# Kernel tuning notes

Hardware: AMD Instinct MI355X
Metric: run time of the kernel (lower is better)

## Reference

```python
import jax, jax.numpy as jnp
import numpy as np

D_MODEL = 1024
N_HEADS = 16
D_K = D_MODEL // N_HEADS
D_FF = 4096
B = 2
T = 2048


def _layernorm(x, gamma, beta, eps=1e-5):
    mu = jnp.mean(x, axis=-1, keepdims=True)
    var = jnp.var(x, axis=-1, keepdims=True)
    return (x - mu) * jax.lax.rsqrt(var + eps) * gamma + beta


def _attention(q_in, kv_in, Wq, bq, Wk, bk, Wv, bv, mask):
    # q_in: [B,Tq,D], kv_in: [B,Tk,D]; Wq/Wk/Wv: [H,D,d_k]; b*: [H,d_k]
    Q = jnp.einsum('btd,hdk->bhtk', q_in, Wq) + bq[None, :, None, :]
    K = jnp.einsum('bsd,hdk->bhsk', kv_in, Wk) + bk[None, :, None, :]
    V = jnp.einsum('bsd,hdk->bhsk', kv_in, Wv) + bv[None, :, None, :]
    scores = jnp.einsum('bhtk,bhsk->bhts', Q, K) / jnp.sqrt(jnp.asarray(D_K, Q.dtype))
    if mask is not None:
        scores = jnp.where(mask, scores, jnp.finfo(scores.dtype).min)
    attn = jax.nn.softmax(scores, axis=-1)
    out = jnp.einsum('bhts,bhsk->bhtk', attn, V)  # [B,H,Tq,d_k]
    # concat heads: [B,Tq,H*d_k] == [B,Tq,D]
    return out.transpose(0, 2, 1, 3).reshape(q_in.shape[0], q_in.shape[1], -1)


def setup_inputs() -> dict:
    key = jax.random.key(0)
    ks = jax.random.split(key, 24)
    s = 0.02
    inp = {
        'dec_input': jax.random.normal(ks[0], (B, T, D_MODEL), jnp.float32),
        'enc_output': jax.random.normal(ks[1], (B, T, D_MODEL), jnp.float32),
        # self-attention per-head weights stacked over heads
        'Wq_s': jax.random.normal(ks[2], (N_HEADS, D_MODEL, D_K), jnp.float32) * s,
        'bq_s': jnp.zeros((N_HEADS, D_K), jnp.float32),
        'Wk_s': jax.random.normal(ks[3], (N_HEADS, D_MODEL, D_K), jnp.float32) * s,
        'bk_s': jnp.zeros((N_HEADS, D_K), jnp.float32),
        'Wv_s': jax.random.normal(ks[4], (N_HEADS, D_MODEL, D_K), jnp.float32) * s,
        'bv_s': jnp.zeros((N_HEADS, D_K), jnp.float32),
        'Wo_s': jax.random.normal(ks[5], (D_MODEL, D_MODEL), jnp.float32) * s,
        'bo_s': jnp.zeros((D_MODEL,), jnp.float32),
        # cross-attention per-head weights
        'Wq_c': jax.random.normal(ks[6], (N_HEADS, D_MODEL, D_K), jnp.float32) * s,
        'bq_c': jnp.zeros((N_HEADS, D_K), jnp.float32),
        'Wk_c': jax.random.normal(ks[7], (N_HEADS, D_MODEL, D_K), jnp.float32) * s,
        'bk_c': jnp.zeros((N_HEADS, D_K), jnp.float32),
        'Wv_c': jax.random.normal(ks[8], (N_HEADS, D_MODEL, D_K), jnp.float32) * s,
        'bv_c': jnp.zeros((N_HEADS, D_K), jnp.float32),
        'Wo_c': jax.random.normal(ks[9], (D_MODEL, D_MODEL), jnp.float32) * s,
        'bo_c': jnp.zeros((D_MODEL,), jnp.float32),
        # FFN
        'W1': jax.random.normal(ks[10], (D_MODEL, D_FF), jnp.float32) * s,
        'b1': jnp.zeros((D_FF,), jnp.float32),
        'W2': jax.random.normal(ks[11], (D_FF, D_MODEL), jnp.float32) * s,
        'b2': jnp.zeros((D_MODEL,), jnp.float32),
        # layernorms
        'g1': jnp.ones((D_MODEL,), jnp.float32), 'be1': jnp.zeros((D_MODEL,), jnp.float32),
        'g2': jnp.ones((D_MODEL,), jnp.float32), 'be2': jnp.zeros((D_MODEL,), jnp.float32),
        'g3': jnp.ones((D_MODEL,), jnp.float32), 'be3': jnp.zeros((D_MODEL,), jnp.float32),
    }
    return inp


def reference(dec_input, enc_output,
              Wq_s, bq_s, Wk_s, bk_s, Wv_s, bv_s, Wo_s, bo_s,
              Wq_c, bq_c, Wk_c, bk_c, Wv_c, bv_c, Wo_c, bo_c,
              W1, b1, W2, b2, g1, be1, g2, be2, g3, be3):
    Tq = dec_input.shape[1]
    causal = jnp.tril(jnp.ones((Tq, Tq), bool))[None, None, :, :]  # [1,1,T,T]
    # masked multi-head self-attention (dropout is identity in eval)
    sa = _attention(dec_input, dec_input, Wq_s, bq_s, Wk_s, bk_s, Wv_s, bv_s, causal)
    sa = sa @ Wo_s.T if False else jnp.einsum('btd,ed->bte', sa, Wo_s.T) if False else sa @ Wo_s + bo_s
    x1 = _layernorm(dec_input + sa, g1, be1)
    # cross-attention (no mask)
    ca = _attention(x1, enc_output, Wq_c, bq_c, Wk_c, bk_c, Wv_c, bv_c, None)
    ca = ca @ Wo_c + bo_c
    x2 = _layernorm(x1 + ca, g2, be2)
    # FFN
    ffn = jax.nn.relu(x2 @ W1 + b1) @ W2 + b2
    x3 = _layernorm(x2 + ffn, g3, be3)
    return x3
```

## Files before the change

kernel.cpp:

```cpp
#include <hip/hip_runtime.h>
#include <hip/hip_bf16.h>

typedef __attribute__((ext_vector_type(8))) short short8;
typedef __attribute__((ext_vector_type(4))) short short4v;
typedef __attribute__((ext_vector_type(4))) float floatx4;

#define TDIM 2048
#define BDIM 2
#define MROWS (BDIM * TDIM)

#define ASM_VMCNT0() __asm__ volatile("s_waitcnt vmcnt(0)" ::: "memory")
#define ASM_VMCNT2() __asm__ volatile("s_waitcnt vmcnt(2)" ::: "memory")
#define ASM_LGKM0()  __asm__ volatile("s_waitcnt lgkmcnt(0)" ::: "memory")
#define ASM_BARRIER() __asm__ volatile("s_barrier" ::: "memory")

__device__ __forceinline__ floatx4 mfma16(short4v a, short4v b, floatx4 c) {
#if defined(__HIP_DEVICE_COMPILE__)
#if __has_builtin(__builtin_amdgcn_mfma_f32_16x16x16bf16_1k)
    return __builtin_amdgcn_mfma_f32_16x16x16bf16_1k(a, b, c, 0, 0, 0);
#else
    short8 az = {a[0], a[1], a[2], a[3], 0, 0, 0, 0};
    short8 bz = {b[0], b[1], b[2], b[3], 0, 0, 0, 0};
    return __builtin_amdgcn_mfma_f32_16x16x32_bf16(az, bz, c, 0, 0, 0);
#endif
#else
    (void)a; (void)b;
    return c;
#endif
}

__device__ __forceinline__ void gload_lds16(const void* g, void* l) {
    __builtin_amdgcn_global_load_lds((const __attribute__((address_space(1))) void*)g,
                                     (__attribute__((address_space(3))) void*)l, 16, 0, 0);
}

__device__ __forceinline__ short bf16s(float x) {
    __hip_bfloat16 h = __float2bfloat16(x);
    return *(short*)&h;
}

__device__ __forceinline__ float fexp2(float x) {
#if defined(__HIP_DEVICE_COMPILE__)
#if __has_builtin(__builtin_amdgcn_exp2f)
    return __builtin_amdgcn_exp2f(x);
#else
    return exp2f(x);
#endif
#else
    return x;
#endif
}

__global__ __launch_bounds__(256) void cast2_k(const float* __restrict__ a,
                                               const float* __restrict__ b,
                                               __hip_bfloat16* __restrict__ oa,
                                               __hip_bfloat16* __restrict__ ob) {
    const int blk = blockIdx.x;
    const float* in = (blk < 4096) ? a : b;
    __hip_bfloat16* out = (blk < 4096) ? oa : ob;
    const size_t base = (size_t)(blk & 4095) * 1024 + threadIdx.x * 4;
    float4 v = *(const float4*)&in[base];
    out[base + 0] = __float2bfloat16(v.x);
    out[base + 1] = __float2bfloat16(v.y);
    out[base + 2] = __float2bfloat16(v.z);
    out[base + 3] = __float2bfloat16(v.w);
}

__device__ __forceinline__ void t32(float (*tile)[33], const float* __restrict__ in,
                                    __hip_bfloat16* __restrict__ out, int R, int C,
                                    int c0, int r0) {
    const int tx = threadIdx.x & 31, ty = threadIdx.x >> 5;
#pragma unroll
    for (int i = 0; i < 4; ++i)
        tile[ty + 8 * i][tx] = in[(size_t)(r0 + ty + 8 * i) * C + c0 + tx];
    __syncthreads();
#pragma unroll
    for (int i = 0; i < 4; ++i)
        out[(size_t)(c0 + ty + 8 * i) * R + r0 + tx] = __float2bfloat16(tile[tx][ty + 8 * i]);
}

__global__ __launch_bounds__(256) void prep_w_k(
    const float* __restrict__ Wq_s, const float* __restrict__ Wk_s, const float* __restrict__ Wv_s,
    const float* __restrict__ Wq_c, const float* __restrict__ Wk_c, const float* __restrict__ Wv_c,
    const float* __restrict__ Wo_s, const float* __restrict__ Wo_c,
    const float* __restrict__ W1, const float* __restrict__ W2,
    const float* __restrict__ bq_s, const float* __restrict__ bk_s, const float* __restrict__ bv_s,
    const float* __restrict__ bk_c, const float* __restrict__ bv_c,
    __hip_bfloat16* __restrict__ WtQKVs, __hip_bfloat16* __restrict__ WtQc,
    __hip_bfloat16* __restrict__ WtKVc, __hip_bfloat16* __restrict__ WtOs,
    __hip_bfloat16* __restrict__ WtOc, __hip_bfloat16* __restrict__ Wt1,
    __hip_bfloat16* __restrict__ Wt2,
    float* __restrict__ BiasQKVs, float* __restrict__ BiasKVc) {
    __shared__ float tile[32][33];
    const int t = blockIdx.x;
    if (t < 6144) {
        const int seg = t >> 10, tl = t & 1023;
        const float* s;
        __hip_bfloat16* d;
        if (seg == 0) { s = Wq_s; d = WtQKVs; }
        else if (seg == 1) { s = Wk_s; d = WtQKVs + 1048576; }
        else if (seg == 2) { s = Wv_s; d = WtQKVs + 2097152; }
        else if (seg == 3) { s = Wq_c; d = WtQc; }
        else if (seg == 4) { s = Wk_c; d = WtKVc; }
        else { s = Wv_c; d = WtKVc + 1048576; }
        const int slab = tl >> 6, rem = tl & 63;
        t32(tile, s + (size_t)slab * 65536, d + (size_t)slab * 65536, 1024, 64,
            (rem & 1) * 32, (rem >> 1) * 32);
    } else if (t < 8192) {
        const int rem = (t - 6144) & 1023;
        const float* s = (t < 7168) ? Wo_s : Wo_c;
        __hip_bfloat16* d = (t < 7168) ? WtOs : WtOc;
        t32(tile, s, d, 1024, 1024, (rem & 31) * 32, (rem >> 5) * 32);
    } else if (t < 12288) {
        const int rem = t - 8192;
        t32(tile, W1, Wt1, 1024, 4096, (rem & 127) * 32, (rem >> 7) * 32);
    } else if (t < 16384) {
        const int rem = t - 12288;
        t32(tile, W2, Wt2, 4096, 1024, (rem & 31) * 32, (rem >> 5) * 32);
    } else if (t < 16396) {
        const int i = (t - 16384) * 256 + threadIdx.x;
        BiasQKVs[i] = (i < 1024) ? bq_s[i] : (i < 2048 ? bk_s[i - 1024] : bv_s[i - 2048]);
    } else {
        const int i = (t - 16396) * 256 + threadIdx.x;
        BiasKVc[i] = (i < 1024) ? bk_c[i] : bv_c[i - 1024];
    }
}

__device__ __forceinline__ void gemm_core(
    const __hip_bfloat16* __restrict__ A, const __hip_bfloat16* __restrict__ Bt,
    int K, int kBeg, int kLen,
    const float* __restrict__ bias, __hip_bfloat16* __restrict__ C, int ldc,
    float* __restrict__ Pf,
    __hip_bfloat16* __restrict__ Vt, int vt_col0, int relu,
    int m0, int n0, __hip_bfloat16* sm) {
    const int tid = threadIdx.x;
    const int lane = tid & 63, wave = tid >> 6;
    const int quad = lane >> 4, l16 = lane & 15;
    const int wm = (wave >> 1) * 64, wn = (wave & 1) * 64;
    const int lrow = lane >> 3;
    const int gsw = (((lane & 7) ^ lrow)) * 8;
    const int sw7 = l16 & 7;
    const __hip_bfloat16* gA = A + (size_t)(m0 + wave * 32 + lrow) * K + kBeg + gsw;
    const __hip_bfloat16* gB = Bt + (size_t)(n0 + wave * 32 + lrow) * K + kBeg + gsw;
    __hip_bfloat16* lA = sm + wave * 2048;
    __hip_bfloat16* lB = sm + 16384 + wave * 2048;
    floatx4 acc[4][4] = {};
    const int T = kLen >> 6;
#pragma unroll
    for (int i = 0; i < 4; ++i) {
        gload_lds16(gA + (size_t)i * 8 * K, lA + i * 512);
        gload_lds16(gB + (size_t)i * 8 * K, lB + i * 512);
    }
    for (int t = 0; t < T; ++t) {
        ASM_VMCNT0();
        ASM_BARRIER();
        if (t + 1 < T) {
            const int koff = (t + 1) << 6;
            const int b = ((t + 1) & 1) * 8192;
#pragma unroll
            for (int i = 0; i < 4; ++i) {
                gload_lds16(gA + (size_t)i * 8 * K + koff, lA + b + i * 512);
                gload_lds16(gB + (size_t)i * 8 * K + koff, lB + b + i * 512);
            }
        }
        const __hip_bfloat16* cA = sm + (t & 1) * 8192;
        const __hip_bfloat16* cB = sm + 16384 + (t & 1) * 8192;
#pragma unroll
        for (int kc = 0; kc < 2; ++kc) {
            short8 af[4], bfr[4];
#pragma unroll
            for (int i = 0; i < 4; ++i) {
                af[i] = *(const short8*)&cA[(wm + i * 16 + l16) * 64 +
                                            (((kc * 4 + quad) ^ sw7) * 8)];
                bfr[i] = *(const short8*)&cB[(wn + i * 16 + l16) * 64 +
                                             (((kc * 4 + quad) ^ sw7) * 8)];
            }
#pragma unroll
            for (int mi = 0; mi < 4; ++mi)
#pragma unroll
                for (int ni = 0; ni < 4; ++ni)
                    acc[mi][ni] =
                        __builtin_amdgcn_mfma_f32_16x16x32_bf16(af[mi], bfr[ni], acc[mi][ni], 0, 0, 0);
        }
    }
    if (Pf) {
#pragma unroll
        for (int ni = 0; ni < 4; ++ni) {
            const int col = n0 + wn + ni * 16 + l16;
#pragma unroll
            for (int mi = 0; mi < 4; ++mi)
#pragma unroll
                for (int r = 0; r < 4; ++r) {
                    const int row = m0 + wm + mi * 16 + quad * 4 + r;
                    Pf[(size_t)row * ldc + col] = acc[mi][ni][r];
                }
        }
    } else {
        const bool toVt = (n0 >= vt_col0);
#pragma unroll
        for (int ni = 0; ni < 4; ++ni) {
            const int col = n0 + wn + ni * 16 + l16;
            const float bv = bias[col];
#pragma unroll
            for (int mi = 0; mi < 4; ++mi) {
                const int row0 = m0 + wm + mi * 16 + quad * 4;
                if (toVt) {
                    const int b = row0 >> 11, t0 = row0 & (TDIM - 1);
                    short4v pk;
#pragma unroll
                    for (int r = 0; r < 4; ++r) pk[r] = bf16s(acc[mi][ni][r] + bv);
                    *(short4v*)&Vt[((size_t)(b * 1024 + (col - vt_col0)) << 11) + t0] = pk;
                } else {
#pragma unroll
                    for (int r = 0; r < 4; ++r) {
                        float v = acc[mi][ni][r] + bv;
                        if (relu) v = fmaxf(v, 0.f);
                        C[(size_t)(row0 + r) * ldc + col] = __float2bfloat16(v);
                    }
                }
            }
        }
    }
}

__global__ __launch_bounds__(256) void gemm_sk2_k(const __hip_bfloat16* __restrict__ A,
                                                  const __hip_bfloat16* __restrict__ Bt,
                                                  float* __restrict__ Pf, int N, int K) {
    __shared__ __hip_bfloat16 sm[2 * 128 * 64 * 2];
    const int z = blockIdx.z;
    gemm_core(A, Bt, K, z * (K >> 1), K >> 1, nullptr, nullptr, N,
              Pf + (size_t)z * MROWS * N, nullptr, 1 << 30, 0,
              blockIdx.y * 128, blockIdx.x * 128, sm);
}

__device__ __forceinline__ void gemm256_core(
    const __hip_bfloat16* __restrict__ A, const __hip_bfloat16* __restrict__ Bt,
    int K, int kBeg, int kLen,
    const float* __restrict__ bias, __hip_bfloat16* __restrict__ C, int ldc,
    float* __restrict__ Pf,
    __hip_bfloat16* __restrict__ Vt, int vt_col0, int relu,
    int m0, int n0, __hip_bfloat16* sm) {
    const int tid = threadIdx.x;
    const int lane = tid & 63, wave = tid >> 6;
    const int quad = lane >> 4, l16 = lane & 15;
    const int wm = (wave >> 2) * 128, wn = (wave & 3) * 64;
    const int lrow = lane >> 3;
    const int gsw = ((lane & 7) ^ lrow) * 8;
    const int sw7 = l16 & 7;
    const __hip_bfloat16* aSrc = A + (size_t)(m0 + wave * 16 + lrow) * K + kBeg + gsw;
    const __hip_bfloat16* bSrc = Bt + (size_t)(n0 + wave * 16 + lrow) * K + kBeg + gsw;
    floatx4 acc[8][4] = {};
    const int T = kLen >> 6;
#pragma unroll
    for (int h = 0; h < 2; ++h)
#pragma unroll
        for (int j = 0; j < 2; ++j) {
            const size_t ro = (size_t)(h * 128 + j * 8);
            gload_lds16(aSrc + ro * K, sm + (h * 128 + wave * 16 + j * 8) * 64);
            gload_lds16(bSrc + ro * K, sm + 16384 + (h * 128 + wave * 16 + j * 8) * 64);
        }
    for (int t = 0; t < T; ++t) {
        const int c = t & 1;
        const int nt = (t + 1 < T) ? (t + 1) : t;
        const size_t nko = (size_t)nt * 64;
        __hip_bfloat16* dst = sm + (1 - c) * 32768;
        const __hip_bfloat16* cA = sm + c * 32768;
        const __hip_bfloat16* cB = cA + 16384;
        ASM_BARRIER();
#pragma unroll
        for (int j = 0; j < 2; ++j)
            gload_lds16(aSrc + (size_t)(j * 8) * K + nko, dst + (wave * 16 + j * 8) * 64);
        ASM_VMCNT2();
        ASM_BARRIER();
        short8 af[4], bfr[4];
#pragma unroll
        for (int i = 0; i < 4; ++i) {
            af[i] = *(const short8*)&cA[(wm + i * 16 + l16) * 64 + ((quad ^ sw7) * 8)];
            bfr[i] = *(const short8*)&cB[(wn + i * 16 + l16) * 64 + ((quad ^ sw7) * 8)];
        }
        __builtin_amdgcn_s_setprio(1);
#pragma unroll
        for (int mi = 0; mi < 4; ++mi)
#pragma unroll
            for (int ni = 0; ni < 4; ++ni)
                acc[mi][ni] = __builtin_amdgcn_mfma_f32_16x16x32_bf16(af[mi], bfr[ni], acc[mi][ni], 0, 0, 0);
        __builtin_amdgcn_s_setprio(0);
        ASM_BARRIER();
#pragma unroll
        for (int i = 0; i < 4; ++i)
            af[i] = *(const short8*)&cA[(wm + 64 + i * 16 + l16) * 64 + ((quad ^ sw7) * 8)];
#pragma unroll
        for (int j = 0; j < 2; ++j)
            gload_lds16(aSrc + (size_t)(128 + j * 8) * K + nko, dst + (128 + wave * 16 + j * 8) * 64);
        __builtin_amdgcn_s_setprio(1);
#pragma unroll
        for (int mi = 0; mi < 4; ++mi)
#pragma unroll
            for (int ni = 0; ni < 4; ++ni)
                acc[4 + mi][ni] = __builtin_amdgcn_mfma_f32_16x16x32_bf16(af[mi], bfr[ni], acc[4 + mi][ni], 0, 0, 0);
        __builtin_amdgcn_s_setprio(0);
        ASM_BARRIER();
#pragma unroll
        for (int i = 0; i < 4; ++i) {
            af[i] = *(const short8*)&cA[(wm + i * 16 + l16) * 64 + (((4 + quad) ^ sw7) * 8)];
            bfr[i] = *(const short8*)&cB[(wn + i * 16 + l16) * 64 + (((4 + quad) ^ sw7) * 8)];
        }
#pragma unroll
        for (int j = 0; j < 2; ++j)
            gload_lds16(bSrc + (size_t)(j * 8) * K + nko, dst + 16384 + (wave * 16 + j * 8) * 64);
        __builtin_amdgcn_s_setprio(1);
#pragma unroll
        for (int mi = 0; mi < 4; ++mi)
#pragma unroll
            for (int ni = 0; ni < 4; ++ni)
                acc[mi][ni] = __builtin_amdgcn_mfma_f32_16x16x32_bf16(af[mi], bfr[ni], acc[mi][ni], 0, 0, 0);
        __builtin_amdgcn_s_setprio(0);
        ASM_BARRIER();
#pragma unroll
        for (int i = 0; i < 4; ++i)
            af[i] = *(const short8*)&cA[(wm + 64 + i * 16 + l16) * 64 + (((4 + quad) ^ sw7) * 8)];
#pragma unroll
        for (int j = 0; j < 2; ++j)
            gload_lds16(bSrc + (size_t)(128 + j * 8) * K + nko, dst + 16384 + (128 + wave * 16 + j * 8) * 64);
        __builtin_amdgcn_s_setprio(1);
#pragma unroll
        for (int mi = 0; mi < 4; ++mi)
#pragma unroll
            for (int ni = 0; ni < 4; ++ni)
                acc[4 + mi][ni] = __builtin_amdgcn_mfma_f32_16x16x32_bf16(af[mi], bfr[ni], acc[4 + mi][ni], 0, 0, 0);
        __builtin_amdgcn_s_setprio(0);
    }
    if (Pf) {
#pragma unroll
        for (int ni = 0; ni < 4; ++ni) {
            const int col = n0 + wn + ni * 16 + l16;
#pragma unroll
            for (int mi = 0; mi < 8; ++mi)
#pragma unroll
                for (int r = 0; r < 4; ++r) {
                    const int row = m0 + wm + mi * 16 + quad * 4 + r;
                    Pf[(size_t)row * ldc + col] = acc[mi][ni][r];
                }
        }
    } else {
        const bool toVt = (n0 >= vt_col0);
#pragma unroll
        for (int ni = 0; ni < 4; ++ni) {
            const int col = n0 + wn + ni * 16 + l16;
            const float bv = bias[col];
#pragma unroll
            for (int mi = 0; mi < 8; ++mi) {
                const int row0 = m0 + wm + mi * 16 + quad * 4;
                if (toVt) {
                    const int b = row0 >> 11, t0 = row0 & (TDIM - 1);
                    short4v pk;
#pragma unroll
                    for (int r = 0; r < 4; ++r) pk[r] = bf16s(acc[mi][ni][r] + bv);
                    *(short4v*)&Vt[((size_t)(b * 1024 + (col - vt_col0)) << 11) + t0] = pk;
                } else {
#pragma unroll
                    for (int r = 0; r < 4; ++r) {
                        float v = acc[mi][ni][r] + bv;
                        if (relu) v = fmaxf(v, 0.f);
                        C[(size_t)(row0 + r) * ldc + col] = __float2bfloat16(v);
                    }
                }
            }
        }
    }
}

__global__ __launch_bounds__(512, 2) void g256_k(const __hip_bfloat16* __restrict__ A,
                                                 const __hip_bfloat16* __restrict__ Bt,
                                                 const float* __restrict__ bias,
                                                 __hip_bfloat16* __restrict__ C,
                                                 int N, int K, int kSplit, int relu,
                                                 __hip_bfloat16* __restrict__ Vt, int vt_col0,
                                                 float* __restrict__ Pf) {
    __shared__ __hip_bfloat16 sm[65536];
    const int z = blockIdx.z;
    float* pf = Pf ? Pf + (size_t)z * MROWS * N : nullptr;
    gemm256_core(A, Bt, K, z * kSplit, kSplit, bias, C, N, pf, Vt, vt_col0, relu,
                 blockIdx.y * 256, blockIdx.x * 256, sm);
}

__global__ __launch_bounds__(512, 2) void g256_pair_k(
    const __hip_bfloat16* __restrict__ A1, const __hip_bfloat16* __restrict__ Bt1,
    const float* __restrict__ bias1, __hip_bfloat16* __restrict__ C1, int N1, int K1,
    const __hip_bfloat16* __restrict__ A2, const __hip_bfloat16* __restrict__ Bt2,
    const float* __restrict__ bias2, __hip_bfloat16* __restrict__ C2, int N2, int K2,
    __hip_bfloat16* __restrict__ Vt2, int vtc2, int nx1) {
    __shared__ __hip_bfloat16 sm[65536];
    if ((int)blockIdx.x < nx1)
        gemm256_core(A1, Bt1, K1, 0, K1, bias1, C1, N1, nullptr, nullptr, 1 << 30, 0,
                     blockIdx.y * 256, blockIdx.x * 256, sm);
    else
        gemm256_core(A2, Bt2, K2, 0, K2, bias2, C2, N2, nullptr, Vt2, vtc2, 0,
                     blockIdx.y * 256, (blockIdx.x - nx1) * 256, sm);
}

__device__ __forceinline__ void flash_one(
    const __hip_bfloat16* __restrict__ Q, int ldq, int qc0,
    const __hip_bfloat16* __restrict__ Kp, int ldk,
    const __hip_bfloat16* __restrict__ Vp,
    __hip_bfloat16* __restrict__ O, int causal, int q0, size_t rowb, int h,
    int tBeg, int tEnd, float* __restrict__ Opart, float* __restrict__ lpart,
    __hip_bfloat16* sK, __hip_bfloat16* sV) {
    const int tid = threadIdx.x, lane = tid & 63, wave = tid >> 6;
    const int quad = lane >> 4, l16 = lane & 15;
    const int lrow = lane >> 3;
    const int gsw = ((lane & 7) ^ lrow) * 8;
    const int sw7 = l16 & 7;
    short8 qf[2];
    {
        const __hip_bfloat16* qp = Q + (rowb + q0 + wave * 16 + l16) * (size_t)ldq + qc0 + h * 64;
        const float qs = 0.18033688f;
        short8 r0 = *(const short8*)(qp + quad * 8);
        short8 r1 = *(const short8*)(qp + 32 + quad * 8);
#pragma unroll
        for (int j = 0; j < 8; ++j) {
            qf[0][j] = bf16s(__uint_as_float(((unsigned)(unsigned short)r0[j]) << 16) * qs);
            qf[1][j] = bf16s(__uint_as_float(((unsigned)(unsigned short)r1[j]) << 16) * qs);
        }
    }
    short4v ones4;
#pragma unroll
    for (int j = 0; j < 4; ++j) ones4[j] = (short)0x3F80;
    floatx4 Ot[4] = {};
    floatx4 accl = {};
    const int nDiag = q0 >> 6;
    ASM_LGKM0();
    ASM_BARRIER();
    {
        const int s0 = tBeg << 6, pb = (tBeg & 1) * 4096;
#pragma unroll
        for (int i = 0; i < 2; ++i) {
            const int rb = wave * 16 + i * 8;
            gload_lds16(&Kp[(rowb + s0 + rb + lrow) * (size_t)ldk + gsw], &sK[pb + rb * 64]);
            gload_lds16(&Vp[(size_t)(rb + lrow) * TDIM + s0 + gsw], &sV[pb + rb * 64]);
        }
    }
    for (int t = tBeg; t < tEnd; ++t) {
        ASM_VMCNT0();
        ASM_BARRIER();
        if (t + 1 < tEnd) {
            const int s1 = (t + 1) << 6, nb = ((t + 1) & 1) * 4096;
#pragma unroll
            for (int i = 0; i < 2; ++i) {
                const int rb = wave * 16 + i * 8;
                gload_lds16(&Kp[(rowb + s1 + rb + lrow) * (size_t)ldk + gsw], &sK[nb + rb * 64]);
                gload_lds16(&Vp[(size_t)(rb + lrow) * TDIM + s1 + gsw], &sV[nb + rb * 64]);
            }
        }
        const int cb = (t & 1) * 4096;
        floatx4 Sf[4] = {};
#pragma unroll
        for (int st = 0; st < 4; ++st) {
            short8 b0 = *(const short8*)&sK[cb + (st * 16 + l16) * 64 + ((quad ^ sw7) * 8)];
            short8 b1 = *(const short8*)&sK[cb + (st * 16 + l16) * 64 + (((4 + quad) ^ sw7) * 8)];
            Sf[st] = __builtin_amdgcn_mfma_f32_16x16x32_bf16(b0, qf[0], Sf[st], 0, 0, 0);
            Sf[st] = __builtin_amdgcn_mfma_f32_16x16x32_bf16(b1, qf[1], Sf[st], 0, 0, 0);
        }
#pragma unroll
        for (int st = 0; st < 4; ++st)
#pragma unroll
            for (int r = 0; r < 4; ++r) Sf[st][r] = fexp2(Sf[st][r]);
        if (causal && t == nDiag) {
            const int qr = wave * 16 + l16;
#pragma unroll
            for (int st = 0; st < 4; ++st)
#pragma unroll
                for (int r = 0; r < 4; ++r)
                    if (st * 16 + quad * 4 + r > qr) Sf[st][r] = 0.f;
        }
        short4v pf[4];
#pragma unroll
        for (int st = 0; st < 4; ++st)
#pragma unroll
            for (int r = 0; r < 4; ++r) pf[st][r] = bf16s(Sf[st][r]);
#pragma unroll
        for (int st = 0; st < 4; ++st) accl = mfma16(ones4, pf[st], accl);
#pragma unroll
        for (int dt = 0; dt < 4; ++dt)
#pragma unroll
            for (int st = 0; st < 4; ++st) {
                short4v av = *(const short4v*)&sV[cb + (dt * 16 + l16) * 64 +
                                                 (((st * 2 + (quad >> 1)) ^ sw7) * 8) +
                                                 (quad & 1) * 4];
                Ot[dt] = mfma16(av, pf[st], Ot[dt]);
            }
    }
    if (Opart) {
        const int qrow = wave * 16 + l16;
#pragma unroll
        for (int dt = 0; dt < 4; ++dt)
            *(floatx4*)&Opart[qrow * 64 + dt * 16 + quad * 4] = Ot[dt];
        if (quad == 0) lpart[qrow] = accl[0];
    } else {
        const float inv = 1.0f / accl[0];
        __hip_bfloat16* op = O + (rowb + q0 + wave * 16 + l16) * (size_t)1024 + h * 64 + quad * 4;
#pragma unroll
        for (int dt = 0; dt < 4; ++dt) {
            short4v pk;
#pragma unroll
            for (int r = 0; r < 4; ++r) pk[r] = bf16s(Ot[dt][r] * inv);
            *(short4v*)(op + dt * 16) = pk;
        }
    }
}

__global__ __launch_bounds__(256) void flash_attn(const __hip_bfloat16* __restrict__ Q, int ldq, int qc0,
                                                  const __hip_bfloat16* __restrict__ K, int ldk, int kc0,
                                                  const __hip_bfloat16* __restrict__ Vt,
                                                  __hip_bfloat16* __restrict__ O, int causal,
                                                  float* __restrict__ Opart,
                                                  float* __restrict__ lpart) {
    __shared__ __hip_bfloat16 sK[2 * 64 * 64];
    __shared__ __hip_bfloat16 sV[2 * 64 * 64];
    const int bh = blockIdx.y, b = bh >> 4, h = bh & 15;
    const size_t rowb = (size_t)b * TDIM;
    const __hip_bfloat16* Kp = K + kc0 + h * 64;
    const __hip_bfloat16* Vp = Vt + ((size_t)(b * 1024 + h * 64) << 11);
    if (causal) {
        const int bx = blockIdx.x;
        if (bx < 32) {
            const int i = 16 + (bx >> 1), hh = bx & 1;
            const int n = i + 1, n2 = n >> 1;
            const int p = bh * 16 + (i - 16);
            float* Op = Opart + (size_t)p * 8192 + hh * 4096;
            float* lp = lpart + p * 128 + hh * 64;
            flash_one(Q, ldq, qc0, Kp, ldk, Vp, O, 1, i * 64, rowb, h,
                      hh ? n2 : 0, hh ? n : n2, Op, lp, sK, sV);
        } else {
            const int i = 47 - bx;
            flash_one(Q, ldq, qc0, Kp, ldk, Vp, O, 1, i * 64, rowb, h,
                      0, i + 1, nullptr, nullptr, sK, sV);
        }
    } else {
        flash_one(Q, ldq, qc0, Kp, ldk, Vp, O, 0, (int)blockIdx.x * 64, rowb, h,
                  0, TDIM >> 6, nullptr, nullptr, sK, sV);
    }
}

__global__ __launch_bounds__(256) void fa_combine_k(const float* __restrict__ Opart,
                                                    const float* __restrict__ lpart,
                                                    __hip_bfloat16* __restrict__ O) {
    const int p = blockIdx.x;
    const int bh = p >> 4, i = (p & 15) + 16;
    const int b = bh >> 4, h = bh & 15;
    const int tid = threadIdx.x;
    const int q = tid >> 2, dseg = (tid & 3) * 16;
    const float* O0 = Opart + (size_t)p * 8192;
    const float* O1 = O0 + 4096;
    const float inv = 1.f / (lpart[p * 128 + q] + lpart[p * 128 + 64 + q]);
    __hip_bfloat16* op = O + ((size_t)(b * TDIM) + i * 64 + q) * 1024 + h * 64 + dseg;
#pragma unroll
    for (int j = 0; j < 4; ++j) {
        floatx4 a = *(const floatx4*)&O0[q * 64 + dseg + j * 4];
        floatx4 c = *(const floatx4*)&O1[q * 64 + dseg + j * 4];
        short4v pk;
#pragma unroll
        for (int r = 0; r < 4; ++r) pk[r] = bf16s((a[r] + c[r]) * inv);
        *(short4v*)(op + j * 4) = pk;
    }
}

__global__ __launch_bounds__(256) void ln2_k(const float* __restrict__ resid,
                                             const float* __restrict__ d0,
                                             const float* __restrict__ d1,
                                             const float* __restrict__ biasN,
                                             const float* __restrict__ gamma,
                                             const float* __restrict__ beta,
                                             float* __restrict__ outf,
                                             __hip_bfloat16* __restrict__ outb) {
    const int row = blockIdx.x, tid = threadIdx.x;
    const size_t base = (size_t)row * 1024;
    float x[4], s = 0.f, sq = 0.f;
#pragma unroll
    for (int i = 0; i < 4; ++i) {
        const int c = tid + 256 * i;
        x[i] = resid[base + c] + d0[base + c] + d1[base + c] + biasN[c];
        s += x[i];
        sq += x[i] * x[i];
    }
#pragma unroll
    for (int off = 32; off > 0; off >>= 1) {
        s += __shfl_down(s, off);
        sq += __shfl_down(sq, off);
    }
    __shared__ float red[8];
    if ((tid & 63) == 0) {
        red[tid >> 6] = s;
        red[4 + (tid >> 6)] = sq;
    }
    __syncthreads();
    const float S = red[0] + red[1] + red[2] + red[3];
    const float Q2 = red[4] + red[5] + red[6] + red[7];
    const float mean = S * (1.f / 1024.f);
    const float var = Q2 * (1.f / 1024.f) - mean * mean;
    const float rstd = rsqrtf(var + 1e-5f);
#pragma unroll
    for (int i = 0; i < 4; ++i) {
        const int c = tid + 256 * i;
        const float y = (x[i] - mean) * rstd * gamma[c] + beta[c];
        outf[base + c] = y;
        if (outb) outb[base + c] = __float2bfloat16(y);
    }
}

extern "C" void kernel_launch(void* const* d_in, const int* in_sizes, int n_in,
                              void* d_out, int out_size, void* d_ws, size_t ws_size,
                              hipStream_t stream) {
    (void)in_sizes; (void)n_in; (void)out_size; (void)ws_size;
    const float* dec  = (const float*)d_in[0];
    const float* enc  = (const float*)d_in[1];
    const float* Wq_s = (const float*)d_in[2];
    const float* bq_s = (const float*)d_in[3];
    const float* Wk_s = (const float*)d_in[4];
    const float* bk_s = (const float*)d_in[5];
    const float* Wv_s = (const float*)d_in[6];
    const float* bv_s = (const float*)d_in[7];
    const float* Wo_s = (const float*)d_in[8];
    const float* bo_s = (const float*)d_in[9];
    const float* Wq_c = (const float*)d_in[10];
    const float* bq_c = (const float*)d_in[11];
    const float* Wk_c = (const float*)d_in[12];
    const float* bk_c = (const float*)d_in[13];
    const float* Wv_c = (const float*)d_in[14];
    const float* bv_c = (const float*)d_in[15];
    const float* Wo_c = (const float*)d_in[16];
    const float* bo_c = (const float*)d_in[17];
    const float* W1   = (const float*)d_in[18];
    const float* b1   = (const float*)d_in[19];
    const float* W2   = (const float*)d_in[20];
    const float* b2   = (const float*)d_in[21];
    const float* g1   = (const float*)d_in[22];
    const float* be1  = (const float*)d_in[23];
    const float* g2   = (const float*)d_in[24];
    const float* be2  = (const float*)d_in[25];
    const float* g3   = (const float*)d_in[26];
    const float* be3  = (const float*)d_in[27];

    char* w = (char*)d_ws;
    const size_t MB = 1ull << 20;
    __hip_bfloat16* Xdec   = (__hip_bfloat16*)(w + 0 * MB);
    __hip_bfloat16* Xenc   = (__hip_bfloat16*)(w + 8 * MB);
    __hip_bfloat16* WtQKVs = (__hip_bfloat16*)(w + 16 * MB);
    __hip_bfloat16* WtOs   = (__hip_bfloat16*)(w + 22 * MB);
    __hip_bfloat16* WtQc   = (__hip_bfloat16*)(w + 24 * MB);
    __hip_bfloat16* WtKVc  = (__hip_bfloat16*)(w + 26 * MB);
    __hip_bfloat16* WtOc   = (__hip_bfloat16*)(w + 30 * MB);
    __hip_bfloat16* Wt1    = (__hip_bfloat16*)(w + 32 * MB);
    __hip_bfloat16* Wt2    = (__hip_bfloat16*)(w + 40 * MB);
    float*          BiasQKVs = (float*)(w + 48 * MB);
    float*          BiasKVc  = (float*)(w + 48 * MB + 65536);
    __hip_bfloat16* QKV    = (__hip_bfloat16*)(w + 49 * MB);
    __hip_bfloat16* Qc     = QKV;
    __hip_bfloat16* KVc    = (__hip_bfloat16*)(w + 57 * MB);
    float*          Psplit = (float*)(w + 49 * MB);
    __hip_bfloat16* VtBuf  = (__hip_bfloat16*)(w + 73 * MB);
    __hip_bfloat16* Attn   = (__hip_bfloat16*)(w + 81 * MB);
    float*          X1f    = (float*)(w + 97 * MB);
    __hip_bfloat16* X1b    = (__hip_bfloat16*)(w + 113 * MB);
    float*          X2f    = (float*)(w + 121 * MB);
    __hip_bfloat16* X2b    = (__hip_bfloat16*)(w + 137 * MB);
    __hip_bfloat16* H1     = (__hip_bfloat16*)(w + 145 * MB);
    float*          FaO    = (float*)(w + 145 * MB);
    float*          FaL    = (float*)(w + 161 * MB);
    float*          P0     = Psplit;
    float*          P1     = Psplit + (size_t)MROWS * 1024;
    const int NOVT = 1 << 30;

    cast2_k<<<8192, 256, 0, stream>>>(dec, enc, Xdec, Xenc);
    prep_w_k<<<16404, 256, 0, stream>>>(Wq_s, Wk_s, Wv_s, Wq_c, Wk_c, Wv_c, Wo_s, Wo_c,
                                        W1, W2, bq_s, bk_s, bv_s, bk_c, bv_c,
                                        WtQKVs, WtQc, WtKVc, WtOs, WtOc, Wt1, Wt2,
                                        BiasQKVs, BiasKVc);

    g256_k<<<dim3(12, 16, 1), 512, 0, stream>>>(Xdec, WtQKVs, BiasQKVs, QKV, 3072, 1024, 1024, 0,
                                                VtBuf, 2048, nullptr);
    flash_attn<<<dim3(48, 32), 256, 0, stream>>>(QKV, 3072, 0, QKV, 3072, 1024, VtBuf, Attn, 1,
                                                 FaO, FaL);
    fa_combine_k<<<512, 256, 0, stream>>>(FaO, FaL, Attn);
    gemm_sk2_k<<<dim3(8, 32, 2), 256, 0, stream>>>(Attn, WtOs, Psplit, 1024, 1024);
    ln2_k<<<MROWS, 256, 0, stream>>>(dec, P0, P1, bo_s, g1, be1, X1f, X1b);

    g256_pair_k<<<dim3(12, 16, 1), 512, 0, stream>>>(X1b, WtQc, bq_c, Qc, 1024, 1024,
                                                     Xenc, WtKVc, BiasKVc, KVc, 2048, 1024,
                                                     VtBuf, 1024, 4);
    flash_attn<<<dim3(32, 32), 256, 0, stream>>>(Qc, 1024, 0, KVc, 2048, 0, VtBuf, Attn, 0,
                                                 nullptr, nullptr);
    gemm_sk2_k<<<dim3(8, 32, 2), 256, 0, stream>>>(Attn, WtOc, Psplit, 1024, 1024);
    ln2_k<<<MROWS, 256, 0, stream>>>(X1f, P0, P1, bo_c, g2, be2, X2f, X2b);

    g256_k<<<dim3(16, 16, 1), 512, 0, stream>>>(X2b, Wt1, b1, H1, 4096, 1024, 1024, 1,
                                                nullptr, NOVT, nullptr);
    g256_k<<<dim3(4, 16, 2), 512, 0, stream>>>(H1, Wt2, nullptr, nullptr, 1024, 4096, 2048, 0,
                                               nullptr, NOVT, Psplit);
    ln2_k<<<MROWS, 256, 0, stream>>>(X2f, P0, P1, b2, g3, be3, (float*)d_out, (__hip_bfloat16*)nullptr);
}
```

Measured before the change: 533.2 us.

## Simplify GEMM main loop prefetch and use 4-way split-K for FFN down-projection

The 256x256 GEMM main loop drops the interleaved per-quarter prefetch. It now issues all next-tile loads at the start of each iteration, waits with vmcnt(0) and one barrier, and cuts the barriers inside the iteration. The FFN down-projection moves from 2-way to 4-way split-K (128 blocks to 256) to fill more CUs, and a new ln4 kernel sums the four partials plus residual and bias. Waiting on all loads at the top of the loop may expose memory latency. The extra partial buffers reuse workspace regions (offset 0 and X1f), which adds fp32 traffic and relies on those regions being dead at that point.

```diff
diff --git a/kernel.cpp b/kernel.cpp
--- a/kernel.cpp
+++ b/kernel.cpp
@@ -10,7 +10,6 @@
 #define MROWS (BDIM * TDIM)
 
 #define ASM_VMCNT0() __asm__ volatile("s_waitcnt vmcnt(0)" ::: "memory")
-#define ASM_VMCNT2() __asm__ volatile("s_waitcnt vmcnt(2)" ::: "memory")
 #define ASM_LGKM0()  __asm__ volatile("s_waitcnt lgkmcnt(0)" ::: "memory")
 #define ASM_BARRIER() __asm__ volatile("s_barrier" ::: "memory")
 
@@ -261,74 +260,49 @@
         }
     for (int t = 0; t < T; ++t) {
         const int c = t & 1;
-        const int nt = (t + 1 < T) ? (t + 1) : t;
-        const size_t nko = (size_t)nt * 64;
-        __hip_bfloat16* dst = sm + (1 - c) * 32768;
         const __hip_bfloat16* cA = sm + c * 32768;
         const __hip_bfloat16* cB = cA + 16384;
+        ASM_VMCNT0();
         ASM_BARRIER();
-#pragma unroll
-        for (int j = 0; j < 2; ++j)
-            gload_lds16(aSrc + (size_t)(j * 8) * K + nko, dst + (wave * 16 + j * 8) * 64);
-        ASM_VMCNT2();
-        ASM_BARRIER();
-        short8 af[4], bfr[4];
-#pragma unroll
-        for (int i = 0; i < 4; ++i) {
-            af[i] = *(const short8*)&cA[(wm + i * 16 + l16) * 64 + ((quad ^ sw7) * 8)];
-            bfr[i] = *(const short8*)&cB[(wn + i * 16 + l16) * 64 + ((quad ^ sw7) * 8)];
-        }
-        __builtin_amdgcn_s_setprio(1);
-#pragma unroll
-        for (int mi = 0; mi < 4; ++mi)
-#pragma unroll
-            for (int ni = 0; ni < 4; ++ni)
-                acc[mi][ni] = __builtin_amdgcn_mfma_f32_16x16x32_bf16(af[mi], bfr[ni], acc[mi][ni], 0, 0, 0);
-        __builtin_amdgcn_s_setprio(0);
-        ASM_BARRIER();
-#pragma unroll
-        for (int i = 0; i < 4; ++i)
-            af[i] = *(const short8*)&cA[(wm + 64 + i * 16 + l16) * 64 + ((quad ^ sw7) * 8)];
-#pragma unroll
-        for (int j = 0; j < 2; ++j)
-            gload_lds16(aSrc + (size_t)(128 + j * 8) * K + nko, dst + (128 + wave * 16 + j * 8) * 64);
-        __builtin_amdgcn_s_setprio(1);
-#pragma unroll
-        for (int mi = 0; mi < 4; ++mi)
-#pragma unroll
-            for (int ni = 0; ni < 4; ++ni)
-                acc[4 + mi][ni] = __builtin_amdgcn_mfma_f32_16x16x32_bf16(af[mi], bfr[ni], acc[4 + mi][ni], 0, 0, 0);
-        __builtin_amdgcn_s_setprio(0);
-        ASM_BARRIER();
-#pragma unroll
-        for (int i = 0; i < 4; ++i) {
-            af[i] = *(const short8*)&cA[(wm + i * 16 + l16) * 64 + (((4 + quad) ^ sw7) * 8)];
-            bfr[i] = *(const short8*)&cB[(wn + i * 16 + l16) * 64 + (((4 + quad) ^ sw7) * 8)];
-        }
-#pragma unroll
-        for (int j = 0; j < 2; ++j)
-            gload_lds16(bSrc + (size_t)(j * 8) * K + nko, dst + 16384 + (wave * 16 + j * 8) * 64);
-        __builtin_amdgcn_s_setprio(1);
-#pragma unroll
-        for (int mi = 0; mi < 4; ++mi)
-#pragma unroll
-            for (int ni = 0; ni < 4; ++ni)
-                acc[mi][ni] = __builtin_amdgcn_mfma_f32_16x16x32_bf16(af[mi], bfr[ni], acc[mi][ni], 0, 0, 0);
-        __builtin_amdgcn_s_setprio(0);
-        ASM_BARRIER();
-#pragma unroll
-        for (int i = 0; i < 4; ++i)
-            af[i] = *(const short8*)&cA[(wm + 64 + i * 16 + l16) * 64 + (((4 + quad) ^ sw7) * 8)];
-#pragma unroll
-        for (int j = 0; j < 2; ++j)
-            gload_lds16(bSrc + (size_t)(128 + j * 8) * K + nko, dst + 16384 + (128 + wave * 16 + j * 8) * 64);
-        __builtin_amdgcn_s_setprio(1);
-#pragma unroll
-        for (int mi = 0; mi < 4; ++mi)
-#pragma unroll
-            for (int ni = 0; ni < 4; ++ni)
-                acc[4 + mi][ni] = __builtin_amdgcn_mfma_f32_16x16x32_bf16(af[mi], bfr[ni], acc[4 + mi][ni], 0, 0, 0);
-        __builtin_amdgcn_s_setprio(0);
+        if (t + 1 < T) {
+            __hip_bfloat16* dst = sm + (1 - c) * 32768;
+            const size_t nko = (size_t)(t + 1) * 64;
+#pragma unroll
+            for (int h = 0; h < 2; ++h)
+#pragma unroll
+                for (int j = 0; j < 2; ++j) {
+                    const size_t ro = (size_t)(h * 128 + j * 8);
+                    gload_lds16(aSrc + ro * K + nko, dst + (h * 128 + wave * 16 + j * 8) * 64);
+                    gload_lds16(bSrc + ro * K + nko, dst + 16384 + (h * 128 + wave * 16 + j * 8) * 64);
+                }
+        }
+#pragma unroll
+        for (int kh = 0; kh < 2; ++kh) {
+            const int gk = ((kh * 4 + quad) ^ sw7) * 8;
+            short8 af[4], bfr[4];
+#pragma unroll
+            for (int i = 0; i < 4; ++i) {
+                af[i] = *(const short8*)&cA[(wm + i * 16 + l16) * 64 + gk];
+                bfr[i] = *(const short8*)&cB[(wn + i * 16 + l16) * 64 + gk];
+            }
+            __builtin_amdgcn_s_setprio(1);
+#pragma unroll
+            for (int mi = 0; mi < 4; ++mi)
+#pragma unroll
+                for (int ni = 0; ni < 4; ++ni)
+                    acc[mi][ni] = __builtin_amdgcn_mfma_f32_16x16x32_bf16(af[mi], bfr[ni], acc[mi][ni], 0, 0, 0);
+            __builtin_amdgcn_s_setprio(0);
+#pragma unroll
+            for (int i = 0; i < 4; ++i)
+                af[i] = *(const short8*)&cA[(wm + 64 + i * 16 + l16) * 64 + gk];
+            __builtin_amdgcn_s_setprio(1);
+#pragma unroll
+            for (int mi = 0; mi < 4; ++mi)
+#pragma unroll
+                for (int ni = 0; ni < 4; ++ni)
+                    acc[4 + mi][ni] = __builtin_amdgcn_mfma_f32_16x16x32_bf16(af[mi], bfr[ni], acc[4 + mi][ni], 0, 0, 0);
+            __builtin_amdgcn_s_setprio(0);
+        }
     }
     if (Pf) {
 #pragma unroll
@@ -374,14 +348,23 @@
                                                  const __hip_bfloat16* __restrict__ Bt,
                                                  const float* __restrict__ bias,
                                                  __hip_bfloat16* __restrict__ C,
-                                                 int N, int K, int kSplit, int relu,
-                                                 __hip_bfloat16* __restrict__ Vt, int vt_col0,
-                                                 float* __restrict__ Pf) {
+                                                 int N, int K, int relu,
+                                                 __hip_bfloat16* __restrict__ Vt, int vt_col0) {
+    __shared__ __hip_bfloat16 sm[65536];
+    gemm256_core(A, Bt, K, 0, K, bias, C, N, nullptr, Vt, vt_col0, relu,
+                 blockIdx.y * 256, blockIdx.x * 256, sm);
+}
+
+__global__ __launch_bounds__(512, 2) void g256_sk4_k(const __hip_bfloat16* __restrict__ A,
+                                                     const __hip_bfloat16* __restrict__ Bt,
+                                                     float* __restrict__ Pf0, float* __restrict__ Pf1,
+                                                     float* __restrict__ Pf2, float* __restrict__ Pf3,
+                                                     int N, int K) {
     __shared__ __hip_bfloat16 sm[65536];
     const int z = blockIdx.z;
-    float* pf = Pf ? Pf + (size_t)z * MROWS * N : nullptr;
-    gemm256_core(A, Bt, K, z * kSplit, kSplit, bias, C, N, pf, Vt, vt_col0, relu,
-                 blockIdx.y * 256, blockIdx.x * 256, sm);
+    float* pf = (z == 0) ? Pf0 : (z == 1) ? Pf1 : (z == 2) ? Pf2 : Pf3;
+    gemm256_core(A, Bt, K, z * (K >> 2), K >> 2, nullptr, nullptr, N, pf,
+                 nullptr, 1 << 30, 0, blockIdx.y * 256, blockIdx.x * 256, sm);
 }
 
 __global__ __launch_bounds__(512, 2) void g256_pair_k(
@@ -605,6 +588,49 @@
         const float y = (x[i] - mean) * rstd * gamma[c] + beta[c];
         outf[base + c] = y;
         if (outb) outb[base + c] = __float2bfloat16(y);
+    }
+}
+
+__global__ __launch_bounds__(256) void ln4_k(const float* __restrict__ resid,
+                                             const float* __restrict__ d0,
+                                             const float* __restrict__ d1,
+                                             const float* __restrict__ d2,
+                                             const float* __restrict__ d3,
+                                             const float* __restrict__ biasN,
+                                             const float* __restrict__ gamma,
+                                             const float* __restrict__ beta,
+                                             float* __restrict__ outf) {
+    const int row = blockIdx.x, tid = threadIdx.x;
+    const size_t base = (size_t)row * 1024;
+    float x[4], s = 0.f, sq = 0.f;
+#pragma unroll
+    for (int i = 0; i < 4; ++i) {
+        const int c = tid + 256 * i;
+        x[i] = resid[base + c] + d0[base + c] + d1[base + c] + d2[base + c] +
+               d3[base + c] + biasN[c];
+        s += x[i];
+        sq += x[i] * x[i];
+    }
+#pragma unroll
+    for (int off = 32; off > 0; off >>= 1) {
+        s += __shfl_down(s, off);
+        sq += __shfl_down(sq, off);
+    }
+    __shared__ float red[8];
+    if ((tid & 63) == 0) {
+        red[tid >> 6] = s;
+        red[4 + (tid >> 6)] = sq;
+    }
+    __syncthreads();
+    const float S = red[0] + red[1] + red[2] + red[3];
+    const float Q2 = red[4] + red[5] + red[6] + red[7];
+    const float mean = S * (1.f / 1024.f);
+    const float var = Q2 * (1.f / 1024.f) - mean * mean;
+    const float rstd = rsqrtf(var + 1e-5f);
+#pragma unroll
+    for (int i = 0; i < 4; ++i) {
+        const int c = tid + 256 * i;
+        outf[base + c] = (x[i] - mean) * rstd * gamma[c] + beta[c];
     }
 }
 
@@ -669,6 +695,8 @@
     float*          FaL    = (float*)(w + 161 * MB);
     float*          P0     = Psplit;
     float*          P1     = Psplit + (size_t)MROWS * 1024;
+    float*          P2     = (float*)(w + 0 * MB);
+    float*          P3     = X1f;
     const int NOVT = 1 << 30;
 
     cast2_k<<<8192, 256, 0, stream>>>(dec, enc, Xdec, Xenc);
@@ -677,25 +705,24 @@
                                         WtQKVs, WtQc, WtKVc, WtOs, WtOc, Wt1, Wt2,
                                         BiasQKVs, BiasKVc);
 
-    g256_k<<<dim3(12, 16, 1), 512, 0, stream>>>(Xdec, WtQKVs, BiasQKVs, QKV, 3072, 1024, 1024, 0,
-                                                VtBuf, 2048, nullptr);
+    g256_k<<<dim3(12, 16), 512, 0, stream>>>(Xdec, WtQKVs, BiasQKVs, QKV, 3072, 1024, 0,
+                                             VtBuf, 2048);
     flash_attn<<<dim3(48, 32), 256, 0, stream>>>(QKV, 3072, 0, QKV, 3072, 1024, VtBuf, Attn, 1,
                                                  FaO, FaL);
     fa_combine_k<<<512, 256, 0, stream>>>(FaO, FaL, Attn);
     gemm_sk2_k<<<dim3(8, 32, 2), 256, 0, stream>>>(Attn, WtOs, Psplit, 1024, 1024);
     ln2_k<<<MROWS, 256, 0, stream>>>(dec, P0, P1, bo_s, g1, be1, X1f, X1b);
 
-    g256_pair_k<<<dim3(12, 16, 1), 512, 0, stream>>>(X1b, WtQc, bq_c, Qc, 1024, 1024,
-                                                     Xenc, WtKVc, BiasKVc, KVc, 2048, 1024,
-                                                     VtBuf, 1024, 4);
+    g256_pair_k<<<dim3(12, 16), 512, 0, stream>>>(X1b, WtQc, bq_c, Qc, 1024, 1024,
+                                                  Xenc, WtKVc, BiasKVc, KVc, 2048, 1024,
+                                                  VtBuf, 1024, 4);
     flash_attn<<<dim3(32, 32), 256, 0, stream>>>(Qc, 1024, 0, KVc, 2048, 0, VtBuf, Attn, 0,
                                                  nullptr, nullptr);
     gemm_sk2_k<<<dim3(8, 32, 2), 256, 0, stream>>>(Attn, WtOc, Psplit, 1024, 1024);
     ln2_k<<<MROWS, 256, 0, stream>>>(X1f, P0, P1, bo_c, g2, be2, X2f, X2b);
 
-    g256_k<<<dim3(16, 16, 1), 512, 0, stream>>>(X2b, Wt1, b1, H1, 4096, 1024, 1024, 1,
-                                                nullptr, NOVT, nullptr);
-    g256_k<<<dim3(4, 16, 2), 512, 0, stream>>>(H1, Wt2, nullptr, nullptr, 1024, 4096, 2048, 0,
-                                               nullptr, NOVT, Psplit);
-    ln2_k<<<MROWS, 256, 0, stream>>>(X2f, P0, P1, b2, g3, be3, (float*)d_out, (__hip_bfloat16*)nullptr);
-}
+    g256_k<<<dim3(16, 16), 512, 0, stream>>>(X2b, Wt1, b1, H1, 4096, 1024, 1,
+                                             nullptr, NOVT);
+    g256_sk4_k<<<dim3(4, 16, 4), 512, 0, stream>>>(H1, Wt2, P0, P1, P2, P3, 1024, 4096);
+    ln4_k<<<MROWS, 256, 0, stream>>>(X2f, P0, P1, P2, P3, b2, g3, be3, (float*)d_out);
+}
```

Result: faster. 519.8 us (-2.5%).
